# Performance work log

Hardware: AMD Instinct MI355X
Metric: run time of the kernel (lower is better)

Reference implementation:

```python
import jax, jax.numpy as jnp
import numpy as np

EPS = 1e-5

def avg_pool3s2(x):
    # AvgPool2d(kernel=3, stride=2, no padding) on NCHW
    s = jax.lax.reduce_window(x, 0.0, jax.lax.add, (1, 1, 3, 3), (1, 1, 2, 2), 'VALID')
    return s / 9.0

def conv1x1(x, W):
    # x: [n,c,h,w], W: [out,c]
    return jnp.einsum('nchw,oc->nohw', x, W)

def batchnorm(x, g, b):
    # training-mode BN over (N,H,W), biased variance (matches torch normalization)
    m = x.mean(axis=(0, 2, 3), keepdims=True)
    v = x.var(axis=(0, 2, 3), keepdims=True)
    return (x - m) * jax.lax.rsqrt(v + EPS) * g[None, :, None, None] + b[None, :, None, None]

def coord_features(hp, wp):
    # [8, hp, wp]: xmin, ymin, xmax, ymax, xctr, yctr, 1/W, 1/H
    w = jnp.arange(wp, dtype=jnp.float32)
    h = jnp.arange(hp, dtype=jnp.float32)
    xmin = w / wp * 2 - 1
    xmax = (w + 1) / wp * 2 - 1
    xctr = (xmin + xmax) / 2
    ymin = h / hp * 2 - 1
    ymax = (h + 1) / hp * 2 - 1
    yctr = (ymin + ymax) / 2
    bx = lambda a: jnp.broadcast_to(a[None, :], (hp, wp))
    by = lambda a: jnp.broadcast_to(a[:, None], (hp, wp))
    const = lambda v: jnp.full((hp, wp), v, dtype=jnp.float32)
    return jnp.stack([bx(xmin), by(ymin), bx(xmax), by(ymax), bx(xctr), by(yctr),
                      const(1.0 / wp), const(1.0 / hp)], axis=0)

def resize_bilinear_ac(x, H, W):
    # bilinear upsample with align_corners=True, x: [n,c,h,w]
    h, w = x.shape[2], x.shape[3]
    ys = jnp.linspace(0.0, h - 1.0, H)
    xs = jnp.linspace(0.0, w - 1.0, W)
    y0 = jnp.floor(ys).astype(jnp.int32); y1 = jnp.minimum(y0 + 1, h - 1); wy = (ys - y0)[None, None, :, None]
    x0 = jnp.floor(xs).astype(jnp.int32); x1 = jnp.minimum(x0 + 1, w - 1); wx = (xs - x0)[None, None, None, :]
    rows = x[:, :, y0, :] * (1 - wy) + x[:, :, y1, :] * wy          # [n,c,H,w]
    return rows[:, :, :, x0] * (1 - wx) + rows[:, :, :, x1] * wx    # [n,c,H,W]

def setup_inputs() -> dict:
    key = jax.random.key(0)
    ks = jax.random.split(key, 8)
    n, in_dim, hid, h, w = 4, 256, 10, 129, 129
    d = hid + 8  # 18
    return {
        'p_fea': jax.random.normal(ks[0], (n, in_dim, h, w), dtype=jnp.float32),
        'hu': jax.random.normal(ks[1], (n, hid, h, w), dtype=jnp.float32),
        'Wq': jax.random.normal(ks[2], (d, d), dtype=jnp.float32) * 0.05,
        'Wk': jax.random.normal(ks[3], (d, in_dim + 8), dtype=jnp.float32) * 0.05,
        'Wv': jax.random.normal(ks[4], (128, in_dim), dtype=jnp.float32) * 0.05,
        'g_v': jnp.ones((128,), dtype=jnp.float32),
        'b_v': jnp.zeros((128,), dtype=jnp.float32),
        'Wp': jax.random.normal(ks[5], (hid, 128), dtype=jnp.float32) * 0.05,
        'g_p': jnp.ones((hid,), dtype=jnp.float32),
        'b_p': jnp.zeros((hid,), dtype=jnp.float32),
    }

def reference(p_fea, hu, Wq, Wk, Wv, g_v, b_v, Wp, g_p, b_p):
    n, c, h, w = p_fea.shape
    p = avg_pool3s2(p_fea)   # [n,256,hp,wp]
    u = avg_pool3s2(hu)      # [n,10,hp,wp]
    hp, wp = p.shape[2], p.shape[3]
    L = hp * wp
    coord = jnp.broadcast_to(coord_features(hp, wp)[None], (n, 8, hp, wp))
    query = conv1x1(jnp.concatenate([u, coord], axis=1), Wq).reshape(n, -1, L).transpose(0, 2, 1)  # [n,L,18]
    key_t = conv1x1(jnp.concatenate([p, coord], axis=1), Wk).reshape(n, -1, L)                      # [n,18,L]
    val = jax.nn.relu(batchnorm(conv1x1(p, Wv), g_v, b_v)).reshape(n, 128, L)                       # [n,128,L]
    energy = jnp.einsum('nlc,ncm->nlm', query, key_t)            # [n,L,L]
    attn = jax.nn.softmax(energy, axis=-1)
    ctx = jnp.einsum('ncm,nlm->ncl', val, attn).reshape(n, 128, hp, wp)
    ctx = jax.nn.relu(batchnorm(conv1x1(ctx, Wp), g_p, b_p))     # [n,10,hp,wp]
    return resize_bilinear_ac(ctx, h, w)                          # [n,10,h,w]
```

## Files before the change

kernel.cpp:

```cpp
#include <hip/hip_runtime.h>
#include <hip/hip_bf16.h>
#include <cstdint>

#define NN   4
#define LL   4096
#define DD   18
#define CVV  128
#define CIN  256
#define CUU  10
#define HH   129
#define COO  10

typedef unsigned short ushort_t;
typedef __attribute__((ext_vector_type(8))) short short8v;
typedef __attribute__((ext_vector_type(4))) float f32x4;

#define P_OFF    ((size_t)0)
#define U_OFF    ((size_t)4194304)
#define VP_OFF   ((size_t)4358144)
#define QT_OFF   ((size_t)6455296)
#define KT_OFF   ((size_t)6717440)
#define VT_OFF   ((size_t)6979584)
#define VSC_OFF  ((size_t)8028160)
#define VSH_OFF  ((size_t)8028288)
#define S2_OFF   ((size_t)8028416)
#define SH2_OFF  ((size_t)8028432)
#define PART_OFF ((size_t)8028448)
#define KMAX_OFF ((size_t)8030496)

static __device__ __forceinline__ ushort_t f2bf(float x) {
    unsigned int u = __float_as_uint(x);
    unsigned int r = (u + 0x7fffu + ((u >> 16) & 1u)) >> 16;
    return (ushort_t)r;
}

static __device__ __forceinline__ void gload16(const void* g, void* l) {
    __builtin_amdgcn_global_load_lds(
        (const __attribute__((address_space(1))) void*)g,
        (__attribute__((address_space(3))) void*)l, 16, 0, 0);
}

__global__ __launch_bounds__(256) void pool2_kernel(const float* __restrict__ src,
                                                    float* __restrict__ dst,
                                                    int* __restrict__ kz) {
    if (kz != nullptr && blockIdx.x == 0 && threadIdx.x < 128) kz[threadIdx.x] = 0;
    int b = blockIdx.x;
    int plane = b >> 4;
    int rg = b & 15;
    __shared__ float rows[9][132];
    const float* sp = src + (size_t)plane * (HH * HH) + (size_t)(rg * 8) * HH;
    #pragma unroll
    for (int j = 0; j < 9; ++j) {
        if (threadIdx.x < HH) rows[j][threadIdx.x] = sp[(size_t)j * HH + threadIdx.x];
    }
    __syncthreads();
    int row = threadIdx.x >> 6, ow = threadIdx.x & 63;
    const float* r0 = rows[2 * row];
    const float* r1 = rows[2 * row + 1];
    const float* r2 = rows[2 * row + 2];
    int x = 2 * ow;
    float sum = r0[x] + r0[x + 1] + r0[x + 2]
              + r1[x] + r1[x + 1] + r1[x + 2]
              + r2[x] + r2[x + 1] + r2[x + 2];
    dst[(size_t)plane * 4096 + (size_t)(rg * 4 + row) * 64 + ow] = sum * (1.0f / 9.0f);
}

__global__ __launch_bounds__(256) void qk2_kernel(const float* __restrict__ p,
                                                  const float* __restrict__ u,
                                                  const float* __restrict__ Wq,
                                                  const float* __restrict__ Wk,
                                                  ushort_t* __restrict__ qt,
                                                  char* __restrict__ kt_c,
                                                  int* __restrict__ kmaxb) {
    int n = blockIdx.x >> 6;
    int mb = blockIdx.x & 63;
    int tid = threadIdx.x;
    int mloc = tid & 63;
    int cs = tid >> 6;
    int m = mb * 64 + mloc;
    int hi = m >> 6, wi = m & 63;

    __shared__ float kacc[4][64][21];

    float coord[8];
    coord[0] = wi * (2.0f / 64.0f) - 1.0f;
    coord[1] = hi * (2.0f / 64.0f) - 1.0f;
    coord[2] = (wi + 1) * (2.0f / 64.0f) - 1.0f;
    coord[3] = (hi + 1) * (2.0f / 64.0f) - 1.0f;
    coord[4] = 0.5f * (coord[0] + coord[2]);
    coord[5] = 0.5f * (coord[1] + coord[3]);
    coord[6] = 1.0f / 64.0f;
    coord[7] = 1.0f / 64.0f;

    {
        float acc[DD];
        #pragma unroll
        for (int o = 0; o < DD; ++o) acc[o] = 0.0f;
        const float* pc = p + ((size_t)(n * CIN + cs * 64)) * LL + m;
        for (int c0 = 0; c0 < 64; ++c0) {
            float pv = pc[(size_t)c0 * LL];
            const float* wr = Wk + (cs * 64 + c0);
            #pragma unroll
            for (int o = 0; o < DD; ++o) acc[o] = fmaf(pv, wr[o * 264], acc[o]);
        }
        if (cs == 3) {
            #pragma unroll
            for (int j = 0; j < 8; ++j) {
                float cv = coord[j];
                #pragma unroll
                for (int o = 0; o < DD; ++o) acc[o] = fmaf(cv, Wk[o * 264 + CIN + j], acc[o]);
            }
        }
        #pragma unroll
        for (int o = 0; o < DD; ++o) kacc[cs][mloc][o] = acc[o];
    }
    if (cs == 0) {
        float acc[DD];
        #pragma unroll
        for (int o = 0; o < DD; ++o) acc[o] = 0.0f;
        for (int cq = 0; cq < CUU; ++cq) {
            float uv = u[((size_t)(n * CUU + cq)) * LL + m];
            #pragma unroll
            for (int o = 0; o < DD; ++o) acc[o] = fmaf(uv, Wq[o * DD + cq], acc[o]);
        }
        #pragma unroll
        for (int j = 0; j < 8; ++j) {
            float cv = coord[j];
            #pragma unroll
            for (int o = 0; o < DD; ++o) acc[o] = fmaf(cv, Wq[o * DD + CUU + j], acc[o]);
        }
        union { short8v v[4]; ushort_t s[32]; } pk;
        #pragma unroll
        for (int o = 0; o < 32; ++o) pk.s[o] = (o < DD) ? f2bf(acc[o]) : (ushort_t)0;
        short8v* qrow = (short8v*)(qt + ((size_t)(n * LL) + m) * 32);
        #pragma unroll
        for (int j = 0; j < 4; ++j) qrow[j] = pk.v[j];
    }
    __syncthreads();
    {
        int j = cs;
        union { short8v v; ushort_t s[8]; } pk;
        #pragma unroll
        for (int i = 0; i < 8; ++i) {
            int o = j * 8 + i;
            float v = 0.0f;
            if (o < DD)
                v = kacc[0][mloc][o] + kacc[1][mloc][o] + kacc[2][mloc][o] + kacc[3][mloc][o];
            pk.s[i] = (o < DD) ? f2bf(v) : (ushort_t)0;
        }
        int byte = ((mloc << 6) | (j << 4)) ^ (((mloc >> 1) & 7) << 4);
        *(short8v*)(kt_c + (size_t)n * 262144 + (size_t)mb * 4096 + byte) = pk.v;

        int mb8[8];
        #pragma unroll
        for (int i = 0; i < 8; ++i) mb8[i] = (int)(pk.s[i] & 0x7fffu);
        #pragma unroll
        for (int off = 1; off < 64; off <<= 1) {
            #pragma unroll
            for (int i = 0; i < 8; ++i) {
                int ov = __shfl_xor(mb8[i], off);
                mb8[i] = max(mb8[i], ov);
            }
        }
        if (mloc == 0) {
            #pragma unroll
            for (int i = 0; i < 8; ++i)
                atomicMax(&kmaxb[n * 32 + cs * 8 + i], mb8[i] << 16);
        }
    }
}

__global__ __launch_bounds__(256, 2) void val_gemm2_kernel(const float* __restrict__ p,
                                                           const float* __restrict__ Wv,
                                                           float* __restrict__ val_pre) {
    int b = blockIdx.x;
    int n  = b >> 7;
    int cb = (b >> 5) & 3;
    int mb = b & 31;
    int tid = threadIdx.x;
    int cg = tid >> 5;
    int mg = tid & 31;
    int ch0 = cb * 32;
    int m0 = mb * 128;

    __shared__ float Wt[256][36];

    {
        int c4 = tid & 63;
        int chq = tid >> 6;
        #pragma unroll
        for (int j = 0; j < 8; ++j) {
            int ch = chq * 8 + j;
            float4 v = *(const float4*)&Wv[(size_t)(ch0 + ch) * CIN + c4 * 4];
            Wt[c4 * 4 + 0][ch] = v.x;
            Wt[c4 * 4 + 1][ch] = v.y;
            Wt[c4 * 4 + 2][ch] = v.z;
            Wt[c4 * 4 + 3][ch] = v.w;
        }
    }
    __syncthreads();

    const float* pb = p + (size_t)n * CIN * LL + m0 + mg * 4;
    f32x4 a0 = {0.f,0.f,0.f,0.f}, a1 = {0.f,0.f,0.f,0.f};
    f32x4 a2 = {0.f,0.f,0.f,0.f}, a3 = {0.f,0.f,0.f,0.f};

    #pragma unroll 4
    for (int c = 0; c < CIN; ++c) {
        f32x4 pv = *(const f32x4*)(pb + (size_t)c * LL);
        f32x4 wv = *(const f32x4*)&Wt[c][cg * 4];
        a0 += pv * wv.x;
        a1 += pv * wv.y;
        a2 += pv * wv.z;
        a3 += pv * wv.w;
    }

    size_t out = ((size_t)(n * CVV + ch0 + cg * 4)) * LL + m0 + mg * 4;
    *(f32x4*)&val_pre[out]           = a0;
    *(f32x4*)&val_pre[out + LL]      = a1;
    *(f32x4*)&val_pre[out + 2 * LL]  = a2;
    *(f32x4*)&val_pre[out + 3 * LL]  = a3;
}

__global__ __launch_bounds__(256) void bn_partial_kernel(const float* __restrict__ src,
                                                         float* __restrict__ part, int C) {
    int ch = blockIdx.x >> 3;
    int s = blockIdx.x & 7;
    int n = s >> 1;
    int m0 = (s & 1) * 2048 + threadIdx.x * 8;
    const float* b = src + ((size_t)(n * C + ch)) * LL + m0;
    float4 a = *(const float4*)b;
    float4 d = *(const float4*)(b + 4);
    float s1 = a.x + a.y + a.z + a.w + d.x + d.y + d.z + d.w;
    float s2 = a.x*a.x + a.y*a.y + a.z*a.z + a.w*a.w
             + d.x*d.x + d.y*d.y + d.z*d.z + d.w*d.w;

    __shared__ float rs[4], rs2[4];
    #pragma unroll
    for (int off = 32; off; off >>= 1) {
        s1 += __shfl_down(s1, off);
        s2 += __shfl_down(s2, off);
    }
    int wid = threadIdx.x >> 6;
    if ((threadIdx.x & 63) == 0) { rs[wid] = s1; rs2[wid] = s2; }
    __syncthreads();
    if (threadIdx.x == 0) {
        part[(size_t)blockIdx.x * 2]     = rs[0] + rs[1] + rs[2] + rs[3];
        part[(size_t)blockIdx.x * 2 + 1] = rs2[0] + rs2[1] + rs2[2] + rs2[3];
    }
}

__global__ __launch_bounds__(128) void bn_finalize_kernel(const float* __restrict__ part,
                                                          const float* __restrict__ g,
                                                          const float* __restrict__ bta,
                                                          float* __restrict__ scale,
                                                          float* __restrict__ shift, int C) {
    int ch = threadIdx.x;
    if (ch >= C) return;
    float s1 = 0.0f, s2 = 0.0f;
    #pragma unroll
    for (int s = 0; s < 8; ++s) {
        s1 += part[(size_t)(ch * 8 + s) * 2];
        s2 += part[(size_t)(ch * 8 + s) * 2 + 1];
    }
    float mean = s1 * (1.0f / (NN * LL));
    float var = s2 * (1.0f / (NN * LL)) - mean * mean;
    float inv = rsqrtf(var + 1e-5f);
    float sc = g[ch] * inv;
    scale[ch] = sc;
    shift[ch] = bta[ch] - mean * sc;
}

__global__ __launch_bounds__(256) void bn_apply_kernel(const float* __restrict__ val_pre,
                                                       const float* __restrict__ scale,
                                                       const float* __restrict__ shift,
                                                       char* __restrict__ vt_c) {
    int t = blockIdx.x * 256 + threadIdx.x;
    int mq = t & 511;
    int ch = (t >> 9) & 127;
    int n = t >> 16;
    int m0 = mq * 8;
    const float* b = val_pre + ((size_t)(n * CVV + ch)) * LL + m0;
    float4 a = *(const float4*)b;
    float4 d = *(const float4*)(b + 4);
    float sc = scale[ch], sh = shift[ch];
    union { short8v v; ushort_t s[8]; } pk;
    pk.s[0] = f2bf(fmaxf(fmaf(a.x, sc, sh), 0.0f));
    pk.s[1] = f2bf(fmaxf(fmaf(a.y, sc, sh), 0.0f));
    pk.s[2] = f2bf(fmaxf(fmaf(a.z, sc, sh), 0.0f));
    pk.s[3] = f2bf(fmaxf(fmaf(a.w, sc, sh), 0.0f));
    pk.s[4] = f2bf(fmaxf(fmaf(d.x, sc, sh), 0.0f));
    pk.s[5] = f2bf(fmaxf(fmaf(d.y, sc, sh), 0.0f));
    pk.s[6] = f2bf(fmaxf(fmaf(d.z, sc, sh), 0.0f));
    pk.s[7] = f2bf(fmaxf(fmaf(d.w, sc, sh), 0.0f));
    int tile = m0 >> 6, mloc = m0 & 63;
    size_t byte = (size_t)n * 1048576 + (size_t)tile * 16384
                + (size_t)(((ch << 7) | (mloc << 1)) ^ ((ch & 7) << 4));
    *(short8v*)(vt_c + byte) = pk.v;
}

struct PW { ushort_t p[16][72]; };

__global__ __launch_bounds__(256, 2) void attn_proj_kernel(const ushort_t* __restrict__ qt,
                                                           const char* __restrict__ kt_c,
                                                           const char* __restrict__ vt_c,
                                                           const int* __restrict__ kmaxb,
                                                           const float* __restrict__ Wp,
                                                           float* __restrict__ ypart,
                                                           float* __restrict__ Lp) {
    int orig = blockIdx.x;
    int bid = ((orig & 7) << 6) | (orig >> 3);
    int qb = bid & 63;
    int sM = (bid >> 6) & 1;
    int n = bid >> 7;
    int tid = threadIdx.x;
    int w = tid >> 6, lane = tid & 63, c = lane & 15, g = lane >> 4;
    int l0w = qb * 64 + w * 16;

    __shared__ __align__(16) ushort_t K_t[2][2048];
    __shared__ __align__(16) ushort_t V_t[2][8192];
    __shared__ PW pws[4];
    __shared__ float Wpl[COO][CVV];

    for (int i = tid; i < COO * CVV; i += 256) Wpl[i >> 7][i & 127] = Wp[i];

    const char* ktb = kt_c + (size_t)n * 262144;
    const char* vtb = vt_c + (size_t)n * 1048576;
    int tk64 = sM * 32;

    short8v qf = *(const short8v*)(qt + (((size_t)n * LL + l0w + c) << 5) + g * 8);
    int vxor = (c & 7) << 4;

    float bound = 0.0f;
    {
        const int* km = kmaxb + n * 32 + g * 8;
        #pragma unroll
        for (int i = 0; i < 8; ++i) {
            float kv = __int_as_float(km[i]);
            float aq = __uint_as_float(((unsigned int)((ushort_t)qf[i]) & 0x7fffu) << 16);
            bound = fmaf(aq, kv, bound);
        }
        bound += __shfl_xor(bound, 16);
        bound += __shfl_xor(bound, 32);
    }
    float M[4];
    #pragma unroll
    for (int r = 0; r < 4; ++r) M[r] = __shfl(bound, g * 4 + r);

    f32x4 O[8];
    #pragma unroll
    for (int i = 0; i < 8; ++i) O[i] = (f32x4){0.f, 0.f, 0.f, 0.f};
    float Lacc[4] = {0.f, 0.f, 0.f, 0.f};

    {
        const char* ks = ktb + (size_t)tk64 * 4096 + w * 1024 + lane * 16;
        gload16(ks, (char*)K_t[0] + w * 1024);
        const char* vs = vtb + (size_t)tk64 * 16384 + w * 4096 + lane * 16;
        #pragma unroll
        for (int i = 0; i < 4; ++i)
            gload16(vs + i * 1024, (char*)V_t[0] + w * 4096 + i * 1024);
    }
    __syncthreads();
    int buf = 0;
    for (int mt = 0; mt < 32; ++mt) {
        if (mt + 1 < 32) {
            const char* ks = ktb + (size_t)(tk64 + mt + 1) * 4096 + w * 1024 + lane * 16;
            gload16(ks, (char*)K_t[buf ^ 1] + w * 1024);
            const char* vs = vtb + (size_t)(tk64 + mt + 1) * 16384 + w * 4096 + lane * 16;
            #pragma unroll
            for (int i = 0; i < 4; ++i)
                gload16(vs + i * 1024, (char*)V_t[buf ^ 1] + w * 4096 + i * 1024);
        }
        f32x4 S[4];
        const char* kb = (const char*)K_t[buf];
        #pragma unroll
        for (int t = 0; t < 4; ++t) {
            int krow = t * 16 + c;
            int kby = ((krow << 6) | (g << 4)) ^ (((krow >> 1) & 7) << 4);
            short8v kf = *(const short8v*)(kb + kby);
            S[t] = __builtin_amdgcn_mfma_f32_16x16x32_bf16(qf, kf, (f32x4){0.f, 0.f, 0.f, 0.f}, 0, 0, 0);
        }
        #pragma unroll
        for (int t = 0; t < 4; ++t) {
            #pragma unroll
            for (int r = 0; r < 4; ++r) {
                float pv = __expf(S[t][r] - M[r]);
                Lacc[r] += pv;
                pws[w].p[g * 4 + r][t * 16 + c] = f2bf(pv);
            }
        }
        short8v pa0 = *(const short8v*)&pws[w].p[c][g * 8];
        short8v pa1 = *(const short8v*)&pws[w].p[c][32 + g * 8];
        const char* vb = (const char*)V_t[buf];
        __builtin_amdgcn_s_setprio(1);
        #pragma unroll
        for (int ct = 0; ct < 8; ++ct) {
            int row = ct * 16 + c;
            int vby0 = (row << 7) | ((g << 4) ^ vxor);
            int vby1 = (row << 7) | (((1 << 6) | (g << 4)) ^ vxor);
            short8v v0 = *(const short8v*)(vb + vby0);
            short8v v1 = *(const short8v*)(vb + vby1);
            O[ct] = __builtin_amdgcn_mfma_f32_16x16x32_bf16(pa0, v0, O[ct], 0, 0, 0);
            O[ct] = __builtin_amdgcn_mfma_f32_16x16x32_bf16(pa1, v1, O[ct], 0, 0, 0);
        }
        __builtin_amdgcn_s_setprio(0);
        __syncthreads();
        buf ^= 1;
    }
    #pragma unroll
    for (int off = 1; off < 16; off <<= 1) {
        #pragma unroll
        for (int r = 0; r < 4; ++r) Lacc[r] += __shfl_xor(Lacc[r], off);
    }

    float yp[COO][4];
    #pragma unroll
    for (int o = 0; o < COO; ++o)
        #pragma unroll
        for (int r = 0; r < 4; ++r) yp[o][r] = 0.0f;
    #pragma unroll
    for (int ct = 0; ct < 8; ++ct) {
        #pragma unroll
        for (int o = 0; o < COO; ++o) {
            float wv = Wpl[o][ct * 16 + c];
            #pragma unroll
            for (int r = 0; r < 4; ++r)
                yp[o][r] = fmaf(O[ct][r], wv, yp[o][r]);
        }
    }
    #pragma unroll
    for (int off = 1; off < 16; off <<= 1) {
        #pragma unroll
        for (int o = 0; o < COO; ++o)
            #pragma unroll
            for (int r = 0; r < 4; ++r)
                yp[o][r] += __shfl_xor(yp[o][r], off);
    }
    if (c == 0) {
        #pragma unroll
        for (int r = 0; r < 4; ++r) {
            size_t yrow = (size_t)(sM * (NN * LL) + n * LL + l0w + g * 4 + r);
            #pragma unroll
            for (int o = 0; o < COO; ++o)
                ypart[yrow * COO + o] = yp[o][r];
            Lp[yrow] = Lacc[r];
        }
    }
}

__global__ __launch_bounds__(256) void combine_kernel(const float* __restrict__ ypart,
                                                      const float* __restrict__ Lp,
                                                      float* __restrict__ out_pre) {
    int idx = blockIdx.x * 256 + threadIdx.x;
    int n = idx >> 12;
    int l = idx & 4095;
    int nl = n * LL + l;
    float inv = 1.0f / (Lp[nl] + Lp[NN * LL + nl]);
    const float* y0 = ypart + (size_t)nl * COO;
    const float* y1 = ypart + ((size_t)(NN * LL) + nl) * COO;
    #pragma unroll
    for (int o = 0; o < COO; ++o)
        out_pre[((size_t)(n * COO + o)) * LL + l] = (y0[o] + y1[o]) * inv;
}

__global__ __launch_bounds__(256) void resize_kernel(const float* __restrict__ out_pre,
                                                     const float* __restrict__ scale,
                                                     const float* __restrict__ shift,
                                                     float* __restrict__ out,
                                                     int total) {
    int idx = blockIdx.x * 256 + threadIdx.x;
    if (idx >= total) return;
    int ow = idx % HH;
    int t = idx / HH;
    int oh = t % HH;
    int t2 = t / HH;
    int o = t2 % COO;
    int n = t2 / COO;

    const float r = 63.0f / 128.0f;
    float y = oh * r;
    float x = ow * r;
    int y0 = (int)y;
    int x0 = (int)x;
    float wy = y - y0;
    float wx = x - x0;
    int y1 = min(y0 + 1, 63);
    int x1 = min(x0 + 1, 63);

    const float* base = out_pre + ((size_t)(n * COO + o)) * LL;
    float sc = scale[o], sh = shift[o];
    float v00 = fmaxf(fmaf(base[y0 * 64 + x0], sc, sh), 0.0f);
    float v01 = fmaxf(fmaf(base[y0 * 64 + x1], sc, sh), 0.0f);
    float v10 = fmaxf(fmaf(base[y1 * 64 + x0], sc, sh), 0.0f);
    float v11 = fmaxf(fmaf(base[y1 * 64 + x1], sc, sh), 0.0f);
    float top = v00 * (1.0f - wx) + v01 * wx;
    float bot = v10 * (1.0f - wx) + v11 * wx;
    out[idx] = top * (1.0f - wy) + bot * wy;
}

extern "C" void kernel_launch(void* const* d_in, const int* in_sizes, int n_in,
                              void* d_out, int out_size, void* d_ws, size_t ws_size,
                              hipStream_t stream) {
    (void)in_sizes; (void)n_in; (void)out_size; (void)ws_size;
    const float* p_fea = (const float*)d_in[0];
    const float* hu    = (const float*)d_in[1];
    const float* Wq    = (const float*)d_in[2];
    const float* Wk    = (const float*)d_in[3];
    const float* Wv    = (const float*)d_in[4];
    const float* g_v   = (const float*)d_in[5];
    const float* b_v   = (const float*)d_in[6];
    const float* Wp    = (const float*)d_in[7];
    const float* g_p   = (const float*)d_in[8];
    const float* b_p   = (const float*)d_in[9];

    float* ws = (float*)d_ws;
    float*    p       = ws + P_OFF;
    float*    u       = ws + U_OFF;
    float*    val_pre = ws + VP_OFF;
    ushort_t* qtb     = (ushort_t*)(ws + QT_OFF);
    char*     ktb     = (char*)(ws + KT_OFF);
    char*     vtb     = (char*)(ws + VT_OFF);
    float*    out_pre = ws + U_OFF;
    float*    Lpart   = ws + VP_OFF;
    float*    ypart   = ws + VP_OFF + 32768;
    float*    vscale  = ws + VSC_OFF;
    float*    vshift  = ws + VSH_OFF;
    float*    scale2  = ws + S2_OFF;
    float*    shift2  = ws + SH2_OFF;
    float*    part    = ws + PART_OFF;
    int*      kmaxb   = (int*)(ws + KMAX_OFF);

    pool2_kernel<<<NN * CIN * 16, 256, 0, stream>>>(p_fea, p, kmaxb);
    pool2_kernel<<<NN * CUU * 16, 256, 0, stream>>>(hu, u, nullptr);
    qk2_kernel<<<256, 256, 0, stream>>>(p, u, Wq, Wk, qtb, ktb, kmaxb);
    val_gemm2_kernel<<<512, 256, 0, stream>>>(p, Wv, val_pre);
    bn_partial_kernel<<<CVV * 8, 256, 0, stream>>>(val_pre, part, CVV);
    bn_finalize_kernel<<<1, 128, 0, stream>>>(part, g_v, b_v, vscale, vshift, CVV);
    bn_apply_kernel<<<(NN * CVV * 512) / 256, 256, 0, stream>>>(val_pre, vscale, vshift, vtb);
    attn_proj_kernel<<<512, 256, 0, stream>>>(qtb, ktb, vtb, kmaxb, Wp, ypart, Lpart);
    combine_kernel<<<(NN * LL) / 256, 256, 0, stream>>>(ypart, Lpart, out_pre);
    bn_partial_kernel<<<COO * 8, 256, 0, stream>>>(out_pre, part, COO);
    bn_finalize_kernel<<<1, 128, 0, stream>>>(part, g_p, b_p, scale2, shift2, COO);
    {
        int total = NN * COO * HH * HH;
        resize_kernel<<<(total + 255) / 256, 256, 0, stream>>>(out_pre, scale2, shift2,
                                                               (float*)d_out, total);
    }
}
```

Measured before the change: 153.0 us.

## Process two query tiles per wave and split keys four ways in attention

```diff
diff --git a/kernel.cpp b/kernel.cpp
--- a/kernel.cpp
+++ b/kernel.cpp
@@ -298,23 +298,27 @@
     *(short8v*)(vt_c + byte) = pk.v;
 }
 
-struct PW { ushort_t p[16][72]; };
-
-__global__ __launch_bounds__(256, 2) void attn_proj_kernel(const ushort_t* __restrict__ qt,
-                                                           const char* __restrict__ kt_c,
-                                                           const char* __restrict__ vt_c,
-                                                           const int* __restrict__ kmaxb,
-                                                           const float* __restrict__ Wp,
-                                                           float* __restrict__ ypart,
-                                                           float* __restrict__ Lp) {
+struct PW { ushort_t p[2][16][72]; };
+
+__global__ __launch_bounds__(256, 2) void attn_proj2_kernel(const ushort_t* __restrict__ qt,
+                                                            const char* __restrict__ kt_c,
+                                                            const char* __restrict__ vt_c,
+                                                            const int* __restrict__ kmaxb,
+                                                            const float* __restrict__ Wp,
+                                                            float* __restrict__ ypart,
+                                                            float* __restrict__ Lp) {
     int orig = blockIdx.x;
-    int bid = ((orig & 7) << 6) | (orig >> 3);
-    int qb = bid & 63;
-    int sM = (bid >> 6) & 1;
-    int n = bid >> 7;
+    int xcd = orig & 7;
+    int idx = orig >> 3;
+    int qb = idx >> 1;
+    int combo = xcd * 2 + (idx & 1);
+    int n = combo >> 2;
+    int sM = combo & 3;
+    int tk64 = sM * 16;
+
     int tid = threadIdx.x;
     int w = tid >> 6, lane = tid & 63, c = lane & 15, g = lane >> 4;
-    int l0w = qb * 64 + w * 16;
+    int l0w = qb * 128 + w * 32;
 
     __shared__ __align__(16) ushort_t K_t[2][2048];
     __shared__ __align__(16) ushort_t V_t[2][8192];
@@ -325,31 +329,40 @@
 
     const char* ktb = kt_c + (size_t)n * 262144;
     const char* vtb = vt_c + (size_t)n * 1048576;
-    int tk64 = sM * 32;
-
-    short8v qf = *(const short8v*)(qt + (((size_t)n * LL + l0w + c) << 5) + g * 8);
+
+    short8v qfA = *(const short8v*)(qt + (((size_t)n * LL + l0w + c) << 5) + g * 8);
+    short8v qfB = *(const short8v*)(qt + (((size_t)n * LL + l0w + 16 + c) << 5) + g * 8);
     int vxor = (c & 7) << 4;
 
-    float bound = 0.0f;
+    float MA[4], MB[4];
     {
         const int* km = kmaxb + n * 32 + g * 8;
+        float bA = 0.0f, bB = 0.0f;
         #pragma unroll
         for (int i = 0; i < 8; ++i) {
             float kv = __int_as_float(km[i]);
-            float aq = __uint_as_float(((unsigned int)((ushort_t)qf[i]) & 0x7fffu) << 16);
-            bound = fmaf(aq, kv, bound);
-        }
-        bound += __shfl_xor(bound, 16);
-        bound += __shfl_xor(bound, 32);
-    }
-    float M[4];
+            float aA = __uint_as_float(((unsigned int)((ushort_t)qfA[i]) & 0x7fffu) << 16);
+            float aB = __uint_as_float(((unsigned int)((ushort_t)qfB[i]) & 0x7fffu) << 16);
+            bA = fmaf(aA, kv, bA);
+            bB = fmaf(aB, kv, bB);
+        }
+        bA += __shfl_xor(bA, 16); bA += __shfl_xor(bA, 32);
+        bB += __shfl_xor(bB, 16); bB += __shfl_xor(bB, 32);
+        #pragma unroll
+        for (int r = 0; r < 4; ++r) {
+            MA[r] = __shfl(bA, g * 4 + r);
+            MB[r] = __shfl(bB, g * 4 + r);
+        }
+    }
+
+    f32x4 OA[8], OB[8];
     #pragma unroll
-    for (int r = 0; r < 4; ++r) M[r] = __shfl(bound, g * 4 + r);
-
-    f32x4 O[8];
-    #pragma unroll
-    for (int i = 0; i < 8; ++i) O[i] = (f32x4){0.f, 0.f, 0.f, 0.f};
-    float Lacc[4] = {0.f, 0.f, 0.f, 0.f};
+    for (int i = 0; i < 8; ++i) {
+        OA[i] = (f32x4){0.f, 0.f, 0.f, 0.f};
+        OB[i] = (f32x4){0.f, 0.f, 0.f, 0.f};
+    }
+    float LaccA[4] = {0.f, 0.f, 0.f, 0.f};
+    float LaccB[4] = {0.f, 0.f, 0.f, 0.f};
 
     {
         const char* ks = ktb + (size_t)tk64 * 4096 + w * 1024 + lane * 16;
@@ -361,8 +374,8 @@
     }
     __syncthreads();
     int buf = 0;
-    for (int mt = 0; mt < 32; ++mt) {
-        if (mt + 1 < 32) {
+    for (int mt = 0; mt < 16; ++mt) {
+        if (mt + 1 < 16) {
             const char* ks = ktb + (size_t)(tk64 + mt + 1) * 4096 + w * 1024 + lane * 16;
             gload16(ks, (char*)K_t[buf ^ 1] + w * 1024);
             const char* vs = vtb + (size_t)(tk64 + mt + 1) * 16384 + w * 4096 + lane * 16;
@@ -370,26 +383,32 @@
             for (int i = 0; i < 4; ++i)
                 gload16(vs + i * 1024, (char*)V_t[buf ^ 1] + w * 4096 + i * 1024);
         }
-        f32x4 S[4];
+        f32x4 SA[4], SB[4];
         const char* kb = (const char*)K_t[buf];
         #pragma unroll
         for (int t = 0; t < 4; ++t) {
             int krow = t * 16 + c;
             int kby = ((krow << 6) | (g << 4)) ^ (((krow >> 1) & 7) << 4);
             short8v kf = *(const short8v*)(kb + kby);
-            S[t] = __builtin_amdgcn_mfma_f32_16x16x32_bf16(qf, kf, (f32x4){0.f, 0.f, 0.f, 0.f}, 0, 0, 0);
+            SA[t] = __builtin_amdgcn_mfma_f32_16x16x32_bf16(qfA, kf, (f32x4){0.f, 0.f, 0.f, 0.f}, 0, 0, 0);
+            SB[t] = __builtin_amdgcn_mfma_f32_16x16x32_bf16(qfB, kf, (f32x4){0.f, 0.f, 0.f, 0.f}, 0, 0, 0);
         }
         #pragma unroll
         for (int t = 0; t < 4; ++t) {
             #pragma unroll
             for (int r = 0; r < 4; ++r) {
-                float pv = __expf(S[t][r] - M[r]);
-                Lacc[r] += pv;
-                pws[w].p[g * 4 + r][t * 16 + c] = f2bf(pv);
+                float pA = __expf(SA[t][r] - MA[r]);
+                float pB = __expf(SB[t][r] - MB[r]);
+                LaccA[r] += pA;
+                LaccB[r] += pB;
+                pws[w].p[0][g * 4 + r][t * 16 + c] = f2bf(pA);
+                pws[w].p[1][g * 4 + r][t * 16 + c] = f2bf(pB);
             }
         }
-        short8v pa0 = *(const short8v*)&pws[w].p[c][g * 8];
-        short8v pa1 = *(const short8v*)&pws[w].p[c][32 + g * 8];
+        short8v paA0 = *(const short8v*)&pws[w].p[0][c][g * 8];
+        short8v paA1 = *(const short8v*)&pws[w].p[0][c][32 + g * 8];
+        short8v paB0 = *(const short8v*)&pws[w].p[1][c][g * 8];
+        short8v paB1 = *(const short8v*)&pws[w].p[1][c][32 + g * 8];
         const char* vb = (const char*)V_t[buf];
         __builtin_amdgcn_s_setprio(1);
         #pragma unroll
@@ -399,8 +418,10 @@
             int vby1 = (row << 7) | (((1 << 6) | (g << 4)) ^ vxor);
             short8v v0 = *(const short8v*)(vb + vby0);
             short8v v1 = *(const short8v*)(vb + vby1);
-            O[ct] = __builtin_amdgcn_mfma_f32_16x16x32_bf16(pa0, v0, O[ct], 0, 0, 0);
-            O[ct] = __builtin_amdgcn_mfma_f32_16x16x32_bf16(pa1, v1, O[ct], 0, 0, 0);
+            OA[ct] = __builtin_amdgcn_mfma_f32_16x16x32_bf16(paA0, v0, OA[ct], 0, 0, 0);
+            OA[ct] = __builtin_amdgcn_mfma_f32_16x16x32_bf16(paA1, v1, OA[ct], 0, 0, 0);
+            OB[ct] = __builtin_amdgcn_mfma_f32_16x16x32_bf16(paB0, v0, OB[ct], 0, 0, 0);
+            OB[ct] = __builtin_amdgcn_mfma_f32_16x16x32_bf16(paB1, v1, OB[ct], 0, 0, 0);
         }
         __builtin_amdgcn_s_setprio(0);
         __syncthreads();
@@ -409,57 +430,67 @@
     #pragma unroll
     for (int off = 1; off < 16; off <<= 1) {
         #pragma unroll
-        for (int r = 0; r < 4; ++r) Lacc[r] += __shfl_xor(Lacc[r], off);
-    }
-
-    float yp[COO][4];
-    #pragma unroll
-    for (int o = 0; o < COO; ++o)
-        #pragma unroll
-        for (int r = 0; r < 4; ++r) yp[o][r] = 0.0f;
-    #pragma unroll
-    for (int ct = 0; ct < 8; ++ct) {
-        #pragma unroll
-        for (int o = 0; o < COO; ++o) {
-            float wv = Wpl[o][ct * 16 + c];
-            #pragma unroll
-            for (int r = 0; r < 4; ++r)
-                yp[o][r] = fmaf(O[ct][r], wv, yp[o][r]);
-        }
-    }
-    #pragma unroll
-    for (int off = 1; off < 16; off <<= 1) {
+        for (int r = 0; r < 4; ++r) {
+            LaccA[r] += __shfl_xor(LaccA[r], off);
+            LaccB[r] += __shfl_xor(LaccB[r], off);
+        }
+    }
+
+    auto project = [&](const f32x4* O, const float* Lacc, int rowbase) {
+        float yp[COO][4];
         #pragma unroll
         for (int o = 0; o < COO; ++o)
             #pragma unroll
-            for (int r = 0; r < 4; ++r)
-                yp[o][r] += __shfl_xor(yp[o][r], off);
-    }
-    if (c == 0) {
-        #pragma unroll
-        for (int r = 0; r < 4; ++r) {
-            size_t yrow = (size_t)(sM * (NN * LL) + n * LL + l0w + g * 4 + r);
+            for (int r = 0; r < 4; ++r) yp[o][r] = 0.0f;
+        #pragma unroll
+        for (int ct = 0; ct < 8; ++ct) {
+            #pragma unroll
+            for (int o = 0; o < COO; ++o) {
+                float wv = Wpl[o][ct * 16 + c];
+                #pragma unroll
+                for (int r = 0; r < 4; ++r)
+                    yp[o][r] = fmaf(O[ct][r], wv, yp[o][r]);
+            }
+        }
+        #pragma unroll
+        for (int off = 1; off < 16; off <<= 1) {
             #pragma unroll
             for (int o = 0; o < COO; ++o)
-                ypart[yrow * COO + o] = yp[o][r];
-            Lp[yrow] = Lacc[r];
-        }
-    }
-}
-
-__global__ __launch_bounds__(256) void combine_kernel(const float* __restrict__ ypart,
-                                                      const float* __restrict__ Lp,
-                                                      float* __restrict__ out_pre) {
+                #pragma unroll
+                for (int r = 0; r < 4; ++r)
+                    yp[o][r] += __shfl_xor(yp[o][r], off);
+        }
+        if (c == 0) {
+            #pragma unroll
+            for (int r = 0; r < 4; ++r) {
+                size_t yrow = (size_t)(sM * (NN * LL) + n * LL + rowbase + g * 4 + r);
+                #pragma unroll
+                for (int o = 0; o < COO; ++o)
+                    ypart[yrow * COO + o] = yp[o][r];
+                Lp[yrow] = Lacc[r];
+            }
+        }
+    };
+    project(OA, LaccA, l0w);
+    project(OB, LaccB, l0w + 16);
+}
+
+__global__ __launch_bounds__(256) void combine4_kernel(const float* __restrict__ ypart,
+                                                       const float* __restrict__ Lp,
+                                                       float* __restrict__ out_pre) {
     int idx = blockIdx.x * 256 + threadIdx.x;
     int n = idx >> 12;
     int l = idx & 4095;
     int nl = n * LL + l;
-    float inv = 1.0f / (Lp[nl] + Lp[NN * LL + nl]);
+    float den = Lp[nl] + Lp[16384 + nl] + Lp[2 * 16384 + nl] + Lp[3 * 16384 + nl];
+    float inv = 1.0f / den;
     const float* y0 = ypart + (size_t)nl * COO;
-    const float* y1 = ypart + ((size_t)(NN * LL) + nl) * COO;
+    const float* y1 = ypart + ((size_t)(16384) + nl) * COO;
+    const float* y2 = ypart + ((size_t)(2 * 16384) + nl) * COO;
+    const float* y3 = ypart + ((size_t)(3 * 16384) + nl) * COO;
     #pragma unroll
     for (int o = 0; o < COO; ++o)
-        out_pre[((size_t)(n * COO + o)) * LL + l] = (y0[o] + y1[o]) * inv;
+        out_pre[((size_t)(n * COO + o)) * LL + l] = (y0[o] + y1[o] + y2[o] + y3[o]) * inv;
 }
 
 __global__ __launch_bounds__(256) void resize_kernel(const float* __restrict__ out_pre,
@@ -521,7 +552,7 @@
     char*     vtb     = (char*)(ws + VT_OFF);
     float*    out_pre = ws + U_OFF;
     float*    Lpart   = ws + VP_OFF;
-    float*    ypart   = ws + VP_OFF + 32768;
+    float*    ypart   = ws + VP_OFF + 65536;
     float*    vscale  = ws + VSC_OFF;
     float*    vshift  = ws + VSH_OFF;
     float*    scale2  = ws + S2_OFF;
@@ -536,8 +567,8 @@
     bn_partial_kernel<<<CVV * 8, 256, 0, stream>>>(val_pre, part, CVV);
     bn_finalize_kernel<<<1, 128, 0, stream>>>(part, g_v, b_v, vscale, vshift, CVV);
     bn_apply_kernel<<<(NN * CVV * 512) / 256, 256, 0, stream>>>(val_pre, vscale, vshift, vtb);
-    attn_proj_kernel<<<512, 256, 0, stream>>>(qtb, ktb, vtb, kmaxb, Wp, ypart, Lpart);
-    combine_kernel<<<(NN * LL) / 256, 256, 0, stream>>>(ypart, Lpart, out_pre);
+    attn_proj2_kernel<<<512, 256, 0, stream>>>(qtb, ktb, vtb, kmaxb, Wp, ypart, Lpart);
+    combine4_kernel<<<(NN * LL) / 256, 256, 0, stream>>>(ypart, Lpart, out_pre);
     bn_partial_kernel<<<COO * 8, 256, 0, stream>>>(out_pre, part, COO);
     bn_finalize_kernel<<<1, 128, 0, stream>>>(part, g_p, b_p, scale2, shift2, COO);
     {
```

Measured after the change: 153.3 us. Within noise of the previous version (+0.2%).

## Store pooled features and value in bf16, fuse BN statistics into producers

Applied to the files above, without the earlier changes.

```diff
diff --git a/kernel.cpp b/kernel.cpp
--- a/kernel.cpp
+++ b/kernel.cpp
@@ -13,26 +13,31 @@
 
 typedef unsigned short ushort_t;
 typedef __attribute__((ext_vector_type(8))) short short8v;
+typedef __attribute__((ext_vector_type(4))) short short4v;
 typedef __attribute__((ext_vector_type(4))) float f32x4;
 
-#define P_OFF    ((size_t)0)
-#define U_OFF    ((size_t)4194304)
-#define VP_OFF   ((size_t)4358144)
-#define QT_OFF   ((size_t)6455296)
-#define KT_OFF   ((size_t)6717440)
-#define VT_OFF   ((size_t)6979584)
-#define VSC_OFF  ((size_t)8028160)
-#define VSH_OFF  ((size_t)8028288)
-#define S2_OFF   ((size_t)8028416)
-#define SH2_OFF  ((size_t)8028432)
-#define PART_OFF ((size_t)8028448)
-#define KMAX_OFF ((size_t)8030496)
+#define PB_OFF   ((size_t)0)
+#define OP_OFF   ((size_t)2097152)
+#define VAL_OFF  ((size_t)2260992)
+#define QT_OFF   ((size_t)3309568)
+#define KT_OFF   ((size_t)3571712)
+#define VT_OFF   ((size_t)3833856)
+#define VSC_OFF  ((size_t)4882432)
+#define VSH_OFF  ((size_t)4882560)
+#define S2_OFF   ((size_t)4882688)
+#define SH2_OFF  ((size_t)4882704)
+#define PART_OFF ((size_t)4882720)
+#define PART2_OFF ((size_t)4915488)
+#define KMAX_OFF ((size_t)4916768)
 
 static __device__ __forceinline__ ushort_t f2bf(float x) {
     unsigned int u = __float_as_uint(x);
     unsigned int r = (u + 0x7fffu + ((u >> 16) & 1u)) >> 16;
     return (ushort_t)r;
 }
+static __device__ __forceinline__ float bf2f(ushort_t b) {
+    return __uint_as_float(((unsigned int)b) << 16);
+}
 
 static __device__ __forceinline__ void gload16(const void* g, void* l) {
     __builtin_amdgcn_global_load_lds(
@@ -40,9 +45,9 @@
         (__attribute__((address_space(3))) void*)l, 16, 0, 0);
 }
 
-__global__ __launch_bounds__(256) void pool2_kernel(const float* __restrict__ src,
-                                                    float* __restrict__ dst,
-                                                    int* __restrict__ kz) {
+__global__ __launch_bounds__(256) void pool_bf_kernel(const float* __restrict__ src,
+                                                      ushort_t* __restrict__ dst,
+                                                      int* __restrict__ kz) {
     if (kz != nullptr && blockIdx.x == 0 && threadIdx.x < 128) kz[threadIdx.x] = 0;
     int b = blockIdx.x;
     int plane = b >> 4;
@@ -62,16 +67,16 @@
     float sum = r0[x] + r0[x + 1] + r0[x + 2]
               + r1[x] + r1[x + 1] + r1[x + 2]
               + r2[x] + r2[x + 1] + r2[x + 2];
-    dst[(size_t)plane * 4096 + (size_t)(rg * 4 + row) * 64 + ow] = sum * (1.0f / 9.0f);
-}
-
-__global__ __launch_bounds__(256) void qk2_kernel(const float* __restrict__ p,
-                                                  const float* __restrict__ u,
-                                                  const float* __restrict__ Wq,
-                                                  const float* __restrict__ Wk,
-                                                  ushort_t* __restrict__ qt,
-                                                  char* __restrict__ kt_c,
-                                                  int* __restrict__ kmaxb) {
+    dst[(size_t)plane * 4096 + (size_t)(rg * 4 + row) * 64 + ow] = f2bf(sum * (1.0f / 9.0f));
+}
+
+__global__ __launch_bounds__(256) void qk2f_kernel(const ushort_t* __restrict__ pb,
+                                                   const float* __restrict__ hu,
+                                                   const float* __restrict__ Wq,
+                                                   const float* __restrict__ Wk,
+                                                   ushort_t* __restrict__ qt,
+                                                   char* __restrict__ kt_c,
+                                                   int* __restrict__ kmaxb) {
     int n = blockIdx.x >> 6;
     int mb = blockIdx.x & 63;
     int tid = threadIdx.x;
@@ -96,9 +101,9 @@
         float acc[DD];
         #pragma unroll
         for (int o = 0; o < DD; ++o) acc[o] = 0.0f;
-        const float* pc = p + ((size_t)(n * CIN + cs * 64)) * LL + m;
+        const ushort_t* pc = pb + ((size_t)(n * CIN + cs * 64)) * LL + m;
         for (int c0 = 0; c0 < 64; ++c0) {
-            float pv = pc[(size_t)c0 * LL];
+            float pv = bf2f(pc[(size_t)c0 * LL]);
             const float* wr = Wk + (cs * 64 + c0);
             #pragma unroll
             for (int o = 0; o < DD; ++o) acc[o] = fmaf(pv, wr[o * 264], acc[o]);
@@ -118,8 +123,12 @@
         float acc[DD];
         #pragma unroll
         for (int o = 0; o < DD; ++o) acc[o] = 0.0f;
+        const float* hub = hu + ((size_t)(n * CUU)) * (HH * HH) + (size_t)(2 * hi) * HH + 2 * wi;
         for (int cq = 0; cq < CUU; ++cq) {
-            float uv = u[((size_t)(n * CUU + cq)) * LL + m];
+            const float* s = hub + (size_t)cq * (HH * HH);
+            float uv = (s[0] + s[1] + s[2]
+                      + s[HH] + s[HH + 1] + s[HH + 2]
+                      + s[2 * HH] + s[2 * HH + 1] + s[2 * HH + 2]) * (1.0f / 9.0f);
             #pragma unroll
             for (int o = 0; o < DD; ++o) acc[o] = fmaf(uv, Wq[o * DD + cq], acc[o]);
         }
@@ -170,9 +179,10 @@
     }
 }
 
-__global__ __launch_bounds__(256, 2) void val_gemm2_kernel(const float* __restrict__ p,
+__global__ __launch_bounds__(256, 2) void val_gemm3_kernel(const ushort_t* __restrict__ pb,
                                                            const float* __restrict__ Wv,
-                                                           float* __restrict__ val_pre) {
+                                                           ushort_t* __restrict__ val,
+                                                           float* __restrict__ part) {
     int b = blockIdx.x;
     int n  = b >> 7;
     int cb = (b >> 5) & 3;
@@ -200,13 +210,16 @@
     }
     __syncthreads();
 
-    const float* pb = p + (size_t)n * CIN * LL + m0 + mg * 4;
+    const ushort_t* pbb = pb + (size_t)n * CIN * LL + m0 + mg * 4;
     f32x4 a0 = {0.f,0.f,0.f,0.f}, a1 = {0.f,0.f,0.f,0.f};
     f32x4 a2 = {0.f,0.f,0.f,0.f}, a3 = {0.f,0.f,0.f,0.f};
 
     #pragma unroll 4
     for (int c = 0; c < CIN; ++c) {
-        f32x4 pv = *(const f32x4*)(pb + (size_t)c * LL);
+        short4v ps = *(const short4v*)(pbb + (size_t)c * LL);
+        f32x4 pv;
+        pv[0] = bf2f((ushort_t)ps[0]); pv[1] = bf2f((ushort_t)ps[1]);
+        pv[2] = bf2f((ushort_t)ps[2]); pv[3] = bf2f((ushort_t)ps[3]);
         f32x4 wv = *(const f32x4*)&Wt[c][cg * 4];
         a0 += pv * wv.x;
         a1 += pv * wv.y;
@@ -215,52 +228,57 @@
     }
 
     size_t out = ((size_t)(n * CVV + ch0 + cg * 4)) * LL + m0 + mg * 4;
-    *(f32x4*)&val_pre[out]           = a0;
-    *(f32x4*)&val_pre[out + LL]      = a1;
-    *(f32x4*)&val_pre[out + 2 * LL]  = a2;
-    *(f32x4*)&val_pre[out + 3 * LL]  = a3;
-}
-
-__global__ __launch_bounds__(256) void bn_partial_kernel(const float* __restrict__ src,
-                                                         float* __restrict__ part, int C) {
-    int ch = blockIdx.x >> 3;
-    int s = blockIdx.x & 7;
-    int n = s >> 1;
-    int m0 = (s & 1) * 2048 + threadIdx.x * 8;
-    const float* b = src + ((size_t)(n * C + ch)) * LL + m0;
-    float4 a = *(const float4*)b;
-    float4 d = *(const float4*)(b + 4);
-    float s1 = a.x + a.y + a.z + a.w + d.x + d.y + d.z + d.w;
-    float s2 = a.x*a.x + a.y*a.y + a.z*a.z + a.w*a.w
-             + d.x*d.x + d.y*d.y + d.z*d.z + d.w*d.w;
-
-    __shared__ float rs[4], rs2[4];
-    #pragma unroll
-    for (int off = 32; off; off >>= 1) {
-        s1 += __shfl_down(s1, off);
-        s2 += __shfl_down(s2, off);
-    }
-    int wid = threadIdx.x >> 6;
-    if ((threadIdx.x & 63) == 0) { rs[wid] = s1; rs2[wid] = s2; }
-    __syncthreads();
-    if (threadIdx.x == 0) {
-        part[(size_t)blockIdx.x * 2]     = rs[0] + rs[1] + rs[2] + rs[3];
-        part[(size_t)blockIdx.x * 2 + 1] = rs2[0] + rs2[1] + rs2[2] + rs2[3];
-    }
-}
-
-__global__ __launch_bounds__(128) void bn_finalize_kernel(const float* __restrict__ part,
-                                                          const float* __restrict__ g,
-                                                          const float* __restrict__ bta,
-                                                          float* __restrict__ scale,
-                                                          float* __restrict__ shift, int C) {
+    union { short4v v; ushort_t s[4]; } w0, w1, w2, w3;
+    #pragma unroll
+    for (int i = 0; i < 4; ++i) {
+        w0.s[i] = f2bf(a0[i]); w1.s[i] = f2bf(a1[i]);
+        w2.s[i] = f2bf(a2[i]); w3.s[i] = f2bf(a3[i]);
+    }
+    *(short4v*)&val[out]          = w0.v;
+    *(short4v*)&val[out + LL]     = w1.v;
+    *(short4v*)&val[out + 2*LL]   = w2.v;
+    *(short4v*)&val[out + 3*LL]   = w3.v;
+
+    float s1[4], s2[4];
+    s1[0] = a0[0]+a0[1]+a0[2]+a0[3]; s2[0] = a0[0]*a0[0]+a0[1]*a0[1]+a0[2]*a0[2]+a0[3]*a0[3];
+    s1[1] = a1[0]+a1[1]+a1[2]+a1[3]; s2[1] = a1[0]*a1[0]+a1[1]*a1[1]+a1[2]*a1[2]+a1[3]*a1[3];
+    s1[2] = a2[0]+a2[1]+a2[2]+a2[3]; s2[2] = a2[0]*a2[0]+a2[1]*a2[1]+a2[2]*a2[2]+a2[3]*a2[3];
+    s1[3] = a3[0]+a3[1]+a3[2]+a3[3]; s2[3] = a3[0]*a3[0]+a3[1]*a3[1]+a3[2]*a3[2]+a3[3]*a3[3];
+    #pragma unroll
+    for (int off = 1; off < 32; off <<= 1) {
+        #pragma unroll
+        for (int i = 0; i < 4; ++i) {
+            s1[i] += __shfl_xor(s1[i], off);
+            s2[i] += __shfl_xor(s2[i], off);
+        }
+    }
+    if (mg == 0) {
+        #pragma unroll
+        for (int i = 0; i < 4; ++i) {
+            part[(((size_t)b * 8 + cg) * 4 + i) * 2]     = s1[i];
+            part[(((size_t)b * 8 + cg) * 4 + i) * 2 + 1] = s2[i];
+        }
+    }
+}
+
+__global__ __launch_bounds__(128) void bn_finalize_v_kernel(const float* __restrict__ part,
+                                                            const float* __restrict__ g,
+                                                            const float* __restrict__ bta,
+                                                            float* __restrict__ scale,
+                                                            float* __restrict__ shift) {
     int ch = threadIdx.x;
-    if (ch >= C) return;
+    if (ch >= CVV) return;
+    int cb = ch >> 5;
+    int cg = (ch & 31) >> 2;
+    int i = ch & 3;
     float s1 = 0.0f, s2 = 0.0f;
-    #pragma unroll
-    for (int s = 0; s < 8; ++s) {
-        s1 += part[(size_t)(ch * 8 + s) * 2];
-        s2 += part[(size_t)(ch * 8 + s) * 2 + 1];
+    for (int n = 0; n < NN; ++n) {
+        for (int mb = 0; mb < 32; ++mb) {
+            int b = n * 128 + cb * 32 + mb;
+            size_t idx = (((size_t)b * 8 + cg) * 4 + i) * 2;
+            s1 += part[idx];
+            s2 += part[idx + 1];
+        }
     }
     float mean = s1 * (1.0f / (NN * LL));
     float var = s2 * (1.0f / (NN * LL)) - mean * mean;
@@ -270,28 +288,21 @@
     shift[ch] = bta[ch] - mean * sc;
 }
 
-__global__ __launch_bounds__(256) void bn_apply_kernel(const float* __restrict__ val_pre,
-                                                       const float* __restrict__ scale,
-                                                       const float* __restrict__ shift,
-                                                       char* __restrict__ vt_c) {
+__global__ __launch_bounds__(256) void bn_apply2_kernel(const ushort_t* __restrict__ val,
+                                                        const float* __restrict__ scale,
+                                                        const float* __restrict__ shift,
+                                                        char* __restrict__ vt_c) {
     int t = blockIdx.x * 256 + threadIdx.x;
     int mq = t & 511;
     int ch = (t >> 9) & 127;
     int n = t >> 16;
     int m0 = mq * 8;
-    const float* b = val_pre + ((size_t)(n * CVV + ch)) * LL + m0;
-    float4 a = *(const float4*)b;
-    float4 d = *(const float4*)(b + 4);
+    short8v vs = *(const short8v*)(val + ((size_t)(n * CVV + ch)) * LL + m0);
     float sc = scale[ch], sh = shift[ch];
     union { short8v v; ushort_t s[8]; } pk;
-    pk.s[0] = f2bf(fmaxf(fmaf(a.x, sc, sh), 0.0f));
-    pk.s[1] = f2bf(fmaxf(fmaf(a.y, sc, sh), 0.0f));
-    pk.s[2] = f2bf(fmaxf(fmaf(a.z, sc, sh), 0.0f));
-    pk.s[3] = f2bf(fmaxf(fmaf(a.w, sc, sh), 0.0f));
-    pk.s[4] = f2bf(fmaxf(fmaf(d.x, sc, sh), 0.0f));
-    pk.s[5] = f2bf(fmaxf(fmaf(d.y, sc, sh), 0.0f));
-    pk.s[6] = f2bf(fmaxf(fmaf(d.z, sc, sh), 0.0f));
-    pk.s[7] = f2bf(fmaxf(fmaf(d.w, sc, sh), 0.0f));
+    #pragma unroll
+    for (int i = 0; i < 8; ++i)
+        pk.s[i] = f2bf(fmaxf(fmaf(bf2f((ushort_t)vs[i]), sc, sh), 0.0f));
     int tile = m0 >> 6, mloc = m0 & 63;
     size_t byte = (size_t)n * 1048576 + (size_t)tile * 16384
                 + (size_t)(((ch << 7) | (mloc << 1)) ^ ((ch & 7) << 4));
@@ -447,9 +458,10 @@
     }
 }
 
-__global__ __launch_bounds__(256) void combine_kernel(const float* __restrict__ ypart,
-                                                      const float* __restrict__ Lp,
-                                                      float* __restrict__ out_pre) {
+__global__ __launch_bounds__(256) void combine2b_kernel(const float* __restrict__ ypart,
+                                                        const float* __restrict__ Lp,
+                                                        float* __restrict__ out_pre,
+                                                        float* __restrict__ part2) {
     int idx = blockIdx.x * 256 + threadIdx.x;
     int n = idx >> 12;
     int l = idx & 4095;
@@ -457,9 +469,57 @@
     float inv = 1.0f / (Lp[nl] + Lp[NN * LL + nl]);
     const float* y0 = ypart + (size_t)nl * COO;
     const float* y1 = ypart + ((size_t)(NN * LL) + nl) * COO;
-    #pragma unroll
-    for (int o = 0; o < COO; ++o)
-        out_pre[((size_t)(n * COO + o)) * LL + l] = (y0[o] + y1[o]) * inv;
+    float ov[COO];
+    #pragma unroll
+    for (int o = 0; o < COO; ++o) {
+        ov[o] = (y0[o] + y1[o]) * inv;
+        out_pre[((size_t)(n * COO + o)) * LL + l] = ov[o];
+    }
+    float p1[COO], p2[COO];
+    #pragma unroll
+    for (int o = 0; o < COO; ++o) { p1[o] = ov[o]; p2[o] = ov[o] * ov[o]; }
+    #pragma unroll
+    for (int off = 1; off < 64; off <<= 1) {
+        #pragma unroll
+        for (int o = 0; o < COO; ++o) {
+            p1[o] += __shfl_xor(p1[o], off);
+            p2[o] += __shfl_xor(p2[o], off);
+        }
+    }
+    __shared__ float rs1[4][COO], rs2[4][COO];
+    int w = threadIdx.x >> 6, lane = threadIdx.x & 63;
+    if (lane == 0) {
+        #pragma unroll
+        for (int o = 0; o < COO; ++o) { rs1[w][o] = p1[o]; rs2[w][o] = p2[o]; }
+    }
+    __syncthreads();
+    if (threadIdx.x < COO) {
+        int o = threadIdx.x;
+        float a = rs1[0][o] + rs1[1][o] + rs1[2][o] + rs1[3][o];
+        float b = rs2[0][o] + rs2[1][o] + rs2[2][o] + rs2[3][o];
+        part2[((size_t)blockIdx.x * COO + o) * 2]     = a;
+        part2[((size_t)blockIdx.x * COO + o) * 2 + 1] = b;
+    }
+}
+
+__global__ __launch_bounds__(64) void bn_finalize2_kernel(const float* __restrict__ part2,
+                                                          const float* __restrict__ g,
+                                                          const float* __restrict__ bta,
+                                                          float* __restrict__ scale,
+                                                          float* __restrict__ shift) {
+    int ch = threadIdx.x;
+    if (ch >= COO) return;
+    float s1 = 0.0f, s2 = 0.0f;
+    for (int b = 0; b < 64; ++b) {
+        s1 += part2[((size_t)b * COO + ch) * 2];
+        s2 += part2[((size_t)b * COO + ch) * 2 + 1];
+    }
+    float mean = s1 * (1.0f / (NN * LL));
+    float var = s2 * (1.0f / (NN * LL)) - mean * mean;
+    float inv = rsqrtf(var + 1e-5f);
+    float sc = g[ch] * inv;
+    scale[ch] = sc;
+    shift[ch] = bta[ch] - mean * sc;
 }
 
 __global__ __launch_bounds__(256) void resize_kernel(const float* __restrict__ out_pre,
@@ -513,33 +573,30 @@
     const float* b_p   = (const float*)d_in[9];
 
     float* ws = (float*)d_ws;
-    float*    p       = ws + P_OFF;
-    float*    u       = ws + U_OFF;
-    float*    val_pre = ws + VP_OFF;
+    ushort_t* pbb     = (ushort_t*)(ws + PB_OFF);
+    float*    out_pre = ws + OP_OFF;
+    ushort_t* valb    = (ushort_t*)(ws + VAL_OFF);
     ushort_t* qtb     = (ushort_t*)(ws + QT_OFF);
     char*     ktb     = (char*)(ws + KT_OFF);
     char*     vtb     = (char*)(ws + VT_OFF);
-    float*    out_pre = ws + U_OFF;
-    float*    Lpart   = ws + VP_OFF;
-    float*    ypart   = ws + VP_OFF + 32768;
+    float*    Lpart   = ws + VAL_OFF;
+    float*    ypart   = ws + VAL_OFF + 32768;
     float*    vscale  = ws + VSC_OFF;
     float*    vshift  = ws + VSH_OFF;
     float*    scale2  = ws + S2_OFF;
     float*    shift2  = ws + SH2_OFF;
     float*    part    = ws + PART_OFF;
+    float*    part2   = ws + PART2_OFF;
     int*      kmaxb   = (int*)(ws + KMAX_OFF);
 
-    pool2_kernel<<<NN * CIN * 16, 256, 0, stream>>>(p_fea, p, kmaxb);
-    pool2_kernel<<<NN * CUU * 16, 256, 0, stream>>>(hu, u, nullptr);
-    qk2_kernel<<<256, 256, 0, stream>>>(p, u, Wq, Wk, qtb, ktb, kmaxb);
-    val_gemm2_kernel<<<512, 256, 0, stream>>>(p, Wv, val_pre);
-    bn_partial_kernel<<<CVV * 8, 256, 0, stream>>>(val_pre, part, CVV);
-    bn_finalize_kernel<<<1, 128, 0, stream>>>(part, g_v, b_v, vscale, vshift, CVV);
-    bn_apply_kernel<<<(NN * CVV * 512) / 256, 256, 0, stream>>>(val_pre, vscale, vshift, vtb);
+    pool_bf_kernel<<<NN * CIN * 16, 256, 0, stream>>>(p_fea, pbb, kmaxb);
+    qk2f_kernel<<<256, 256, 0, stream>>>(pbb, hu, Wq, Wk, qtb, ktb, kmaxb);
+    val_gemm3_kernel<<<512, 256, 0, stream>>>(pbb, Wv, valb, part);
+    bn_finalize_v_kernel<<<1, 128, 0, stream>>>(part, g_v, b_v, vscale, vshift);
+    bn_apply2_kernel<<<(NN * CVV * 512) / 256, 256, 0, stream>>>(valb, vscale, vshift, vtb);
     attn_proj_kernel<<<512, 256, 0, stream>>>(qtb, ktb, vtb, kmaxb, Wp, ypart, Lpart);
-    combine_kernel<<<(NN * LL) / 256, 256, 0, stream>>>(ypart, Lpart, out_pre);
-    bn_partial_kernel<<<COO * 8, 256, 0, stream>>>(out_pre, part, COO);
-    bn_finalize_kernel<<<1, 128, 0, stream>>>(part, g_p, b_p, scale2, shift2, COO);
+    combine2b_kernel<<<(NN * LL) / 256, 256, 0, stream>>>(ypart, Lpart, out_pre, part2);
+    bn_finalize2_kernel<<<1, 64, 0, stream>>>(part2, g_p, b_p, scale2, shift2);
     {
         int total = NN * COO * HH * HH;
         resize_kernel<<<(total + 255) / 256, 256, 0, stream>>>(out_pre, scale2, shift2,
```

Measured after the change: 155.4 us. Within noise of the previous version (+1.6%).
